# Performance work log

Hardware: AMD Instinct MI355X
Metric: run time of the kernel (lower is better)

Reference implementation:

```python
import jax, jax.numpy as jnp
import numpy as np

B, T, C, H, W = 2, 2048, 2048, 16, 512
D = C // H  # head_dim = 128

def setup_inputs() -> dict:
    key = jax.random.key(0)
    k1, k2, k3 = jax.random.split(key, 3)
    x = jax.random.normal(k1, (B, T, C), dtype=jnp.float32)
    w_attn = jax.random.normal(k2, (C, 3 * C), dtype=jnp.float32) * 0.02
    w_proj = jax.random.normal(k3, (C, C), dtype=jnp.float32) * 0.02
    # standard RoPE tables: [T, D] with halves repeated
    inv_freq = 1.0 / (10000.0 ** (jnp.arange(0, D, 2, dtype=jnp.float32) / D))
    freqs = jnp.outer(jnp.arange(T, dtype=jnp.float32), inv_freq)  # [T, D/2]
    emb = jnp.concatenate([freqs, freqs], axis=-1)  # [T, D]
    return {"x": x, "freqs_cos": jnp.cos(emb), "freqs_sin": jnp.sin(emb),
            "w_attn": w_attn, "w_proj": w_proj}

def _rotate_half(t):
    return jnp.concatenate([-t[..., D // 2:], t[..., :D // 2]], axis=-1)

def reference(x, freqs_cos, freqs_sin, w_attn, w_proj):
    qkv = x @ w_attn  # [B,T,3C]
    q, k, v = jnp.split(qkv, 3, axis=-1)
    # [B,T,C] -> [B,H,T,D]
    q = q.reshape(B, T, H, D).transpose(0, 2, 1, 3)
    k = k.reshape(B, T, H, D).transpose(0, 2, 1, 3)
    v = v.reshape(B, T, H, D).transpose(0, 2, 1, 3)
    cos = freqs_cos[None, None, :, :]  # [1,1,T,D]
    sin = freqs_sin[None, None, :, :]
    q = q * cos + _rotate_half(q) * sin
    k = k * cos + _rotate_half(k) * sin
    scores = jnp.einsum('bhqd,bhkd->bhqk', q, k) / jnp.sqrt(jnp.float32(D))
    i = jnp.arange(T)[:, None]
    j = jnp.arange(T)[None, :]
    band = (j <= i) & (j > i - W)  # causal sliding window of width W
    scores = jnp.where(band[None, None, :, :], scores, -jnp.inf)
    att = jax.nn.softmax(scores, axis=-1)
    y = jnp.einsum('bhqk,bhkd->bhqd', att, v)
    y = y.transpose(0, 2, 1, 3).reshape(B, T, C)
    return y @ w_proj
```

## Files before the change

kernel.cpp:

```cpp
#include <hip/hip_runtime.h>
#include <stdint.h>

#define B_ 2
#define T_ 2048
#define C_ 2048
#define H_ 16
#define D_ 128
#define W_ 512
#define M_ (B_*T_)
#define N1_ (3*C_)

typedef short bf16x8 __attribute__((ext_vector_type(8)));
typedef unsigned short u16x8 __attribute__((ext_vector_type(8)));
typedef float f32x4 __attribute__((ext_vector_type(4)));

#define SB() __builtin_amdgcn_sched_barrier(0)

__device__ __forceinline__ unsigned short f2bf(float f) {
  union { float f; unsigned u; } v; v.f = f;
  unsigned r = v.u + 0x7fffu + ((v.u >> 16) & 1u);
  return (unsigned short)(r >> 16);
}
__device__ __forceinline__ float bf2f(unsigned short b) {
  union { unsigned u; float f; } v; v.u = ((unsigned)b) << 16;
  return v.f;
}

__device__ __forceinline__ void gload_lds16(const void* g, void* l) {
  __builtin_amdgcn_global_load_lds((const __attribute__((address_space(1))) void*)g,
                                   (__attribute__((address_space(3))) void*)l, 16, 0, 0);
}

__global__ void k_cvt(const float* __restrict__ s, unsigned short* __restrict__ d, int n) {
  int i = (blockIdx.x * blockDim.x + threadIdx.x) * 8;
  if (i >= n) return;
  float4 a = *(const float4*)(s + i);
  float4 b = *(const float4*)(s + i + 4);
  u16x8 o;
  o[0]=f2bf(a.x); o[1]=f2bf(a.y); o[2]=f2bf(a.z); o[3]=f2bf(a.w);
  o[4]=f2bf(b.x); o[5]=f2bf(b.y); o[6]=f2bf(b.z); o[7]=f2bf(b.w);
  *(u16x8*)(d + i) = o;
}

__global__ void k_tcvt(const float* __restrict__ s, unsigned short* __restrict__ d, int R, int Cc) {
  __shared__ float tile[32][33];
  int c0 = blockIdx.x * 32, r0 = blockIdx.y * 32;
  int tx = threadIdx.x & 31, ty = threadIdx.x >> 5;
  #pragma unroll
  for (int j = 0; j < 32; j += 8) tile[ty + j][tx] = s[(size_t)(r0 + ty + j) * Cc + c0 + tx];
  __syncthreads();
  #pragma unroll
  for (int j = 0; j < 32; j += 8) d[(size_t)(c0 + ty + j) * R + r0 + tx] = f2bf(tile[tx][ty + j]);
}

template<int ROWS>
__device__ __forceinline__ void stage_half(const unsigned short* __restrict__ gbase,
                                           int row0, int K, int kt, int kh,
                                           unsigned short* region, int tid, int sw) {
  const char* gsrc = (const char*)(gbase + (size_t)row0 * K + kt * 64 + kh * 32);
  {
    int o = tid * 16, s = o ^ sw;
    gload_lds16(gsrc + (size_t)(s >> 6) * (K * 2) + (s & 63), (char*)region + o);
  }
  if (ROWS == 256) {
    int o = (512 + tid) * 16, s = o ^ sw;
    gload_lds16(gsrc + (size_t)(s >> 6) * (K * 2) + (s & 63), (char*)region + o);
  }
}

template<bool F32OUT>
__global__ __launch_bounds__(512, 2) void k_gemm8(const unsigned short* __restrict__ A,
                                                  const unsigned short* __restrict__ Bt,
                                                  void* __restrict__ Cp,
                                                  int Ntot, int K) {
  __shared__ unsigned short As[2][2][256 * 32];
  __shared__ unsigned short Bs[2][2][256 * 32];
  const int tid = threadIdx.x, lane = tid & 63, wv = tid >> 6;
  const int wm = wv >> 2, wn = wv & 3;
  const int lr = lane & 15, lg = lane >> 4;
  const int sw = tid & 32;
  const int fofs = lr * 64 + ((lg * 16) ^ ((lr & 8) << 2));
  const int aoff = wm * 128 * 64 + fofs;
  const int boff = wn * 64 * 64 + fofs;

  const int nwg = gridDim.x;
  const int nbx = Ntot >> 8;
  const int q = nwg >> 3, r = nwg & 7;
  const int xcd = blockIdx.x & 7, off = blockIdx.x >> 3;
  const int bid = (xcd < r ? xcd * (q + 1) : r * (q + 1) + (xcd - r) * q) + off;
  const int bm0 = (bid / nbx) << 8;
  const int bn0 = (bid % nbx) << 8;

  f32x4 acc[8][4];
  #pragma unroll
  for (int i = 0; i < 8; ++i)
    #pragma unroll
    for (int j = 0; j < 4; ++j)
      #pragma unroll
      for (int e = 0; e < 4; ++e) acc[i][j][e] = 0.f;

  const int NT = K >> 6;

  stage_half<256>(A,  bm0, K, 0, 0, As[0][0], tid, sw);
  stage_half<256>(Bt, bn0, K, 0, 0, Bs[0][0], tid, sw);
  stage_half<256>(Bt, bn0, K, 0, 1, Bs[0][1], tid, sw);
  stage_half<256>(A,  bm0, K, 0, 1, As[0][1], tid, sw);
  stage_half<256>(Bt, bn0, K, 1, 0, Bs[1][0], tid, sw);
  stage_half<256>(A,  bm0, K, 1, 0, As[1][0], tid, sw);
  stage_half<256>(Bt, bn0, K, 1, 1, Bs[1][1], tid, sw);
  asm volatile("s_waitcnt vmcnt(4)" ::: "memory");
  __builtin_amdgcn_s_barrier();

  bf16x8 Xa[4], Xb[4], Ya[4];
  #pragma unroll
  for (int j = 0; j < 4; ++j) Xb[j] = *(const bf16x8*)((const char*)Bs[0][0] + boff + j * 1024);
  #pragma unroll
  for (int i = 0; i < 4; ++i) Xa[i] = *(const bf16x8*)((const char*)As[0][0] + aoff + i * 1024);

  #pragma unroll 2
  for (int t = 0; t < NT; ++t) {
    const int p = t & 1;
    asm volatile("s_waitcnt lgkmcnt(0)" ::: "memory");
    __builtin_amdgcn_sched_barrier(0);
    __builtin_amdgcn_s_setprio(1);
    #pragma unroll
    for (int i = 0; i < 4; ++i)
      #pragma unroll
      for (int j = 0; j < 4; ++j)
        acc[i][j] = __builtin_amdgcn_mfma_f32_16x16x32_bf16(Xa[i], Xb[j], acc[i][j], 0, 0, 0);
    __builtin_amdgcn_s_setprio(0);
    #pragma unroll
    for (int i = 0; i < 4; ++i) Ya[i] = *(const bf16x8*)((const char*)As[p][0] + aoff + (i + 4) * 1024);
    if (t + 1 < NT) stage_half<256>(A, bm0, K, t + 1, 1, As[p ^ 1][1], tid, sw);
    __builtin_amdgcn_s_barrier();

    asm volatile("s_waitcnt lgkmcnt(0)" ::: "memory");
    __builtin_amdgcn_sched_barrier(0);
    __builtin_amdgcn_s_setprio(1);
    #pragma unroll
    for (int i = 0; i < 4; ++i)
      #pragma unroll
      for (int j = 0; j < 4; ++j)
        acc[i + 4][j] = __builtin_amdgcn_mfma_f32_16x16x32_bf16(Ya[i], Xb[j], acc[i + 4][j], 0, 0, 0);
    __builtin_amdgcn_s_setprio(0);
    #pragma unroll
    for (int j = 0; j < 4; ++j) Xb[j] = *(const bf16x8*)((const char*)Bs[p][1] + boff + j * 1024);
    #pragma unroll
    for (int i = 0; i < 4; ++i) Xa[i] = *(const bf16x8*)((const char*)As[p][1] + aoff + i * 1024);
    if (t + 2 < NT) stage_half<256>(Bt, bn0, K, t + 2, 0, Bs[p][0], tid, sw);
    __builtin_amdgcn_s_barrier();

    asm volatile("s_waitcnt lgkmcnt(0)" ::: "memory");
    __builtin_amdgcn_sched_barrier(0);
    __builtin_amdgcn_s_setprio(1);
    #pragma unroll
    for (int i = 0; i < 4; ++i)
      #pragma unroll
      for (int j = 0; j < 4; ++j)
        acc[i][j] = __builtin_amdgcn_mfma_f32_16x16x32_bf16(Xa[i], Xb[j], acc[i][j], 0, 0, 0);
    __builtin_amdgcn_s_setprio(0);
    #pragma unroll
    for (int i = 0; i < 4; ++i) Ya[i] = *(const bf16x8*)((const char*)As[p][1] + aoff + (i + 4) * 1024);
    if (t + 2 < NT) stage_half<256>(A, bm0, K, t + 2, 0, As[p][0], tid, sw);
    __builtin_amdgcn_s_barrier();

    asm volatile("s_waitcnt lgkmcnt(0)" ::: "memory");
    __builtin_amdgcn_sched_barrier(0);
    __builtin_amdgcn_s_setprio(1);
    #pragma unroll
    for (int i = 0; i < 4; ++i)
      #pragma unroll
      for (int j = 0; j < 4; ++j)
        acc[i + 4][j] = __builtin_amdgcn_mfma_f32_16x16x32_bf16(Ya[i], Xb[j], acc[i + 4][j], 0, 0, 0);
    __builtin_amdgcn_s_setprio(0);
    if (t < NT - 2) asm volatile("s_waitcnt vmcnt(4)" ::: "memory");
    else            asm volatile("s_waitcnt vmcnt(0)" ::: "memory");
    #pragma unroll
    for (int j = 0; j < 4; ++j) Xb[j] = *(const bf16x8*)((const char*)Bs[p ^ 1][0] + boff + j * 1024);
    #pragma unroll
    for (int i = 0; i < 4; ++i) Xa[i] = *(const bf16x8*)((const char*)As[p ^ 1][0] + aoff + i * 1024);
    if (t + 2 < NT) stage_half<256>(Bt, bn0, K, t + 2, 1, Bs[p][1], tid, sw);
    __builtin_amdgcn_s_barrier();
  }
  asm volatile("s_waitcnt lgkmcnt(0)" ::: "memory");

  #pragma unroll
  for (int i = 0; i < 8; ++i)
    #pragma unroll
    for (int j = 0; j < 4; ++j) {
      int m = bm0 + wm * 128 + i * 16 + lg * 4;
      int n = bn0 + wn * 64 + j * 16 + lr;
      #pragma unroll
      for (int e = 0; e < 4; ++e) {
        if (F32OUT) ((float*)Cp)[(size_t)(m + e) * Ntot + n] = acc[i][j][e];
        else ((unsigned short*)Cp)[(size_t)(m + e) * Ntot + n] = f2bf(acc[i][j][e]);
      }
    }
}

template<bool F32OUT>
__global__ __launch_bounds__(512, 1) void k_gemmT(const unsigned short* __restrict__ A,
                                                  const unsigned short* __restrict__ Bt,
                                                  void* __restrict__ Cp,
                                                  int Ntot, int K) {
  __shared__ unsigned short As[3][2][128 * 32];
  __shared__ unsigned short Bs[3][2][256 * 32];
  const int tid = threadIdx.x, lane = tid & 63, wv = tid >> 6;
  const int wm = wv >> 2, wn = wv & 3;
  const int lr = lane & 15, lg = lane >> 4;
  const int sw = tid & 32;
  const int fofs = lr * 64 + ((lg * 16) ^ ((lr & 8) << 2));
  const int aoff = wm * 64 * 64 + fofs;
  const int boff = wn * 64 * 64 + fofs;

  const int nwg = gridDim.x;
  const int nbx = Ntot >> 8;
  const int q = nwg >> 3, r = nwg & 7;
  const int xcd = blockIdx.x & 7, off = blockIdx.x >> 3;
  const int bid = (xcd < r ? xcd * (q + 1) : r * (q + 1) + (xcd - r) * q) + off;
  const int bm0 = (bid / nbx) * 128;
  const int bn0 = (bid % nbx) << 8;

  f32x4 acc[4][4];
  #pragma unroll
  for (int i = 0; i < 4; ++i)
    #pragma unroll
    for (int j = 0; j < 4; ++j)
      #pragma unroll
      for (int e = 0; e < 4; ++e) acc[i][j][e] = 0.f;

  const int NT = K >> 6;

  auto stage_tile = [&](int kt, int rr) {
    stage_half<128>(A,  bm0, K, kt, 0, As[rr][0], tid, sw);
    stage_half<256>(Bt, bn0, K, kt, 0, Bs[rr][0], tid, sw);
    stage_half<128>(A,  bm0, K, kt, 1, As[rr][1], tid, sw);
    stage_half<256>(Bt, bn0, K, kt, 1, Bs[rr][1], tid, sw);
  };

  stage_tile(0, 0);
  stage_tile(1, 1);
  asm volatile("s_waitcnt vmcnt(6)" ::: "memory");
  __builtin_amdgcn_s_barrier();
  bf16x8 Pf[4], Qf[4], Xf[4], Yf[4];
  #pragma unroll
  for (int i = 0; i < 4; ++i) Pf[i] = *(const bf16x8*)((const char*)As[0][0] + aoff + i * 1024);
  #pragma unroll
  for (int j = 0; j < 4; ++j) Xf[j] = *(const bf16x8*)((const char*)Bs[0][0] + boff + j * 1024);

  int cur = 0;
  for (int t = 0; t < NT; ++t) {
    int rn = cur + 1; if (rn == 3) rn = 0;
    int rs = rn + 1; if (rs == 3) rs = 0;

    asm volatile("s_waitcnt lgkmcnt(0)" ::: "memory");
    SB();
    __builtin_amdgcn_s_setprio(1);
    #pragma unroll
    for (int i = 0; i < 4; ++i)
      #pragma unroll
      for (int j = 0; j < 4; ++j)
        acc[i][j] = __builtin_amdgcn_mfma_f32_16x16x32_bf16(Pf[i], Xf[j], acc[i][j], 0, 0, 0);
    __builtin_amdgcn_s_setprio(0);
    #pragma unroll
    for (int i = 0; i < 4; ++i) Qf[i] = *(const bf16x8*)((const char*)As[cur][1] + aoff + i * 1024);
    #pragma unroll
    for (int j = 0; j < 4; ++j) Yf[j] = *(const bf16x8*)((const char*)Bs[cur][1] + boff + j * 1024);
    if (t + 2 < NT) {
      stage_tile(t + 2, rs);
      asm volatile("s_waitcnt vmcnt(9)" ::: "memory");
    } else if (t + 1 < NT) {
      asm volatile("s_waitcnt vmcnt(3)" ::: "memory");
    } else {
      asm volatile("s_waitcnt vmcnt(0)" ::: "memory");
    }
    __builtin_amdgcn_s_barrier();

    asm volatile("s_waitcnt lgkmcnt(0)" ::: "memory");
    SB();
    __builtin_amdgcn_s_setprio(1);
    #pragma unroll
    for (int i = 0; i < 4; ++i)
      #pragma unroll
      for (int j = 0; j < 4; ++j)
        acc[i][j] = __builtin_amdgcn_mfma_f32_16x16x32_bf16(Qf[i], Yf[j], acc[i][j], 0, 0, 0);
    __builtin_amdgcn_s_setprio(0);
    if (t + 1 < NT) {
      #pragma unroll
      for (int i = 0; i < 4; ++i) Pf[i] = *(const bf16x8*)((const char*)As[rn][0] + aoff + i * 1024);
      #pragma unroll
      for (int j = 0; j < 4; ++j) Xf[j] = *(const bf16x8*)((const char*)Bs[rn][0] + boff + j * 1024);
    }
    if (t + 2 < NT) asm volatile("s_waitcnt vmcnt(6)" ::: "memory");
    else            asm volatile("s_waitcnt vmcnt(0)" ::: "memory");
    __builtin_amdgcn_s_barrier();

    cur = rn;
  }
  asm volatile("s_waitcnt lgkmcnt(0)" ::: "memory");

  #pragma unroll
  for (int i = 0; i < 4; ++i)
    #pragma unroll
    for (int j = 0; j < 4; ++j) {
      int m = bm0 + wm * 64 + i * 16 + lg * 4;
      int n = bn0 + wn * 64 + j * 16 + lr;
      #pragma unroll
      for (int e = 0; e < 4; ++e) {
        if (F32OUT) ((float*)Cp)[(size_t)(m + e) * Ntot + n] = acc[i][j][e];
        else ((unsigned short*)Cp)[(size_t)(m + e) * Ntot + n] = f2bf(acc[i][j][e]);
      }
    }
}

__global__ __launch_bounds__(256) void k_reorg(const unsigned short* __restrict__ qkv,
                        const float* __restrict__ fcos, const float* __restrict__ fsin,
                        unsigned short* __restrict__ q_r, unsigned short* __restrict__ k_r,
                        unsigned short* __restrict__ v_t) {
  const int bh = blockIdx.x, b = bh >> 4, h = bh & 15;
  const int t0 = blockIdx.y * 64;
  const int tid = threadIdx.x;
  __shared__ unsigned short vt[64][136];
  #pragma unroll
  for (int p = 0; p < 4; ++p) {
    int idx = p * 256 + tid;
    int tl = idx >> 4, sg = idx & 15;
    int t = t0 + tl, d0 = sg * 8;
    float sgn = (d0 < 64) ? -1.f : 1.f;
    float4 c0v = *(const float4*)(fcos + t * D_ + d0);
    float4 c1v = *(const float4*)(fcos + t * D_ + d0 + 4);
    float4 s0v = *(const float4*)(fsin + t * D_ + d0);
    float4 s1v = *(const float4*)(fsin + t * D_ + d0 + 4);
    float cs[8] = {c0v.x,c0v.y,c0v.z,c0v.w,c1v.x,c1v.y,c1v.z,c1v.w};
    float sn[8] = {s0v.x,s0v.y,s0v.z,s0v.w,s1v.x,s1v.y,s1v.z,s1v.w};
    #pragma unroll
    for (int w = 0; w < 2; ++w) {
      const unsigned short* src = qkv + (size_t)(b*T_ + t) * N1_ + w*C_ + h*D_;
      u16x8 a  = *(const u16x8*)(src + d0);
      u16x8 pr = *(const u16x8*)(src + (d0 ^ 64));
      u16x8 o;
      #pragma unroll
      for (int e = 0; e < 8; ++e)
        o[e] = f2bf(bf2f(a[e]) * cs[e] + sgn * bf2f(pr[e]) * sn[e]);
      unsigned short* dst = (w ? k_r : q_r) + (size_t)((b*H_ + h)*T_ + t) * D_ + d0;
      *(u16x8*)dst = o;
    }
    const unsigned short* vsrc = qkv + (size_t)(b*T_ + t) * N1_ + 2*C_ + h*D_ + d0;
    *(u16x8*)&vt[tl][d0] = *(const u16x8*)vsrc;
  }
  __syncthreads();
  #pragma unroll
  for (int p = 0; p < 4; ++p) {
    int idx = p * 256 + tid;
    int sg = idx & 7, d = idx >> 3;
    u16x8 o;
    #pragma unroll
    for (int e = 0; e < 8; ++e) o[e] = vt[sg*8 + e][d];
    *(u16x8*)(v_t + (size_t)((b*H_ + h)*D_ + d) * T_ + t0 + sg*8) = o;
  }
}

__global__ __launch_bounds__(512) void k_attn(const unsigned short* __restrict__ q_r,
                       const unsigned short* __restrict__ k_r,
                       const unsigned short* __restrict__ v_t,
                       unsigned short* __restrict__ y) {
  const int bh = blockIdx.x, b = bh >> 4, h = bh & 15;
  const int q0 = blockIdx.y * 128;
  const int tid = threadIdx.x, lane = tid & 63, wv = tid >> 6;
  const int lr = lane & 15, lg = lane >> 4;

  __shared__ unsigned short Ks[2][64 * 128];
  __shared__ unsigned short Vs[2][128 * 64];
  __shared__ unsigned short Ps[8 * 16 * 64];

  const size_t bhT = (size_t)(b*H_ + h) * T_;
  const size_t bhD = (size_t)(b*H_ + h) * D_;
  const unsigned short* qbase = q_r + (bhT + q0 + wv*16 + lr) * D_;
  bf16x8 qf[4];
  #pragma unroll
  for (int kk = 0; kk < 4; ++kk) qf[kk] = *(const bf16x8*)(qbase + kk*32 + lg*8);

  f32x4 o[8];
  #pragma unroll
  for (int i = 0; i < 8; ++i)
    #pragma unroll
    for (int e = 0; e < 4; ++e) o[i][e] = 0.f;
  float m_run[4], l_sum[4];
  #pragma unroll
  for (int e = 0; e < 4; ++e) { m_run[e] = -1e30f; l_sum[e] = 0.f; }

  const int i_min = q0 + wv*16, i_max = i_min + 15;
  int kt_lo = q0 - (W_ - 1); if (kt_lo < 0) kt_lo = 0; kt_lo &= ~63;
  const float scale = 0.08838834764831845f;

  unsigned short* Ps_w = Ps + wv * 1024;

  auto stage_kv = [&](int kt, int buf) {
    #pragma unroll
    for (int c = 0; c < 2; ++c) {
      int ob = (c * 512 + tid) * 16;
      int row = ob >> 8, slot = (ob >> 4) & 15;
      int cb = slot ^ ((row & 7) << 1);
      gload_lds16(k_r + (bhT + kt + row) * D_ + cb * 8, (char*)Ks[buf] + ob);
    }
    #pragma unroll
    for (int c = 0; c < 2; ++c) {
      int ob = (c * 512 + tid) * 16;
      int d = ob >> 7, slot = (ob >> 4) & 7;
      int cb = slot ^ (d & 7);
      gload_lds16(v_t + (bhD + d) * T_ + kt + cb * 8, (char*)Vs[buf] + ob);
    }
  };

  stage_kv(kt_lo, 0);
  int cur = 0;
  for (int kt = kt_lo; kt < q0 + 128; kt += 64) {
    const bool has_next = (kt + 64 < q0 + 128);
    if (has_next) stage_kv(kt + 64, cur ^ 1);
    if (has_next) asm volatile("s_waitcnt vmcnt(4)" ::: "memory");
    else          asm volatile("s_waitcnt vmcnt(0)" ::: "memory");
    __builtin_amdgcn_s_barrier();

    if (kt <= i_max && kt + 63 >= i_min - (W_ - 1)) {
      const unsigned short* Kc = Ks[cur];
      const unsigned short* Vc = Vs[cur];
      f32x4 s[4];
      #pragma unroll
      for (int ct = 0; ct < 4; ++ct)
        #pragma unroll
        for (int e = 0; e < 4; ++e) s[ct][e] = 0.f;
      #pragma unroll
      for (int kk = 0; kk < 4; ++kk) {
        #pragma unroll
        for (int ct = 0; ct < 4; ++ct) {
          bf16x8 kf = *(const bf16x8*)&Kc[(ct*16 + lr)*128 + ((kk*4 + lg) ^ ((lr & 7) << 1))*8];
          s[ct] = __builtin_amdgcn_mfma_f32_16x16x32_bf16(qf[kk], kf, s[ct], 0, 0, 0);
        }
      }
      float sv[4][4], mnew[4];
      int grow = 0;
      #pragma unroll
      for (int e = 0; e < 4; ++e) {
        int i = i_min + lg*4 + e;
        float rm = -1e30f;
        #pragma unroll
        for (int ct = 0; ct < 4; ++ct) {
          int j = kt + ct*16 + lr;
          bool ok = (j <= i) && (j > i - W_);
          sv[e][ct] = ok ? s[ct][e] * scale : -1e30f;
          rm = fmaxf(rm, sv[e][ct]);
        }
        #pragma unroll
        for (int msk = 1; msk < 16; msk <<= 1) rm = fmaxf(rm, __shfl_xor(rm, msk));
        mnew[e] = fmaxf(m_run[e], rm);
        grow |= (mnew[e] > m_run[e]) ? 1 : 0;
      }
      if (__any(grow)) {
        #pragma unroll
        for (int e = 0; e < 4; ++e) {
          float fac = __expf(m_run[e] - mnew[e]);
          l_sum[e] *= fac;
          m_run[e] = mnew[e];
          #pragma unroll
          for (int nt = 0; nt < 8; ++nt) o[nt][e] *= fac;
        }
      }
      #pragma unroll
      for (int e = 0; e < 4; ++e) {
        int prow = lg*4 + e;
        float rs = 0.f;
        #pragma unroll
        for (int ct = 0; ct < 4; ++ct) {
          float pv = (sv[e][ct] > -1e29f) ? __expf(sv[e][ct] - m_run[e]) : 0.f;
          rs += pv;
          Ps_w[prow*64 + ((ct*2 + (lr >> 3)) ^ (prow & 7))*8 + (lr & 7)] = f2bf(pv);
        }
        #pragma unroll
        for (int msk = 1; msk < 16; msk <<= 1) rs += __shfl_xor(rs, msk);
        l_sum[e] += rs;
      }
      asm volatile("s_waitcnt lgkmcnt(0)" ::: "memory"); SB();
      #pragma unroll
      for (int kk = 0; kk < 2; ++kk) {
        bf16x8 pf = *(const bf16x8*)&Ps_w[lr*64 + ((kk*4 + lg) ^ (lr & 7))*8];
        #pragma unroll
        for (int nt = 0; nt < 8; ++nt) {
          bf16x8 vf = *(const bf16x8*)&Vc[(nt*16 + lr)*64 + ((kk*4 + lg) ^ (lr & 7))*8];
          o[nt] = __builtin_amdgcn_mfma_f32_16x16x32_bf16(pf, vf, o[nt], 0, 0, 0);
        }
      }
    }
    asm volatile("s_waitcnt lgkmcnt(0)" ::: "memory");
    __builtin_amdgcn_s_barrier();
    cur ^= 1;
  }

  #pragma unroll
  for (int nt = 0; nt < 8; ++nt) {
    #pragma unroll
    for (int e = 0; e < 4; ++e) {
      int t = q0 + wv*16 + lg*4 + e;
      int d = nt*16 + lr;
      y[(size_t)(b*T_ + t) * C_ + h*D_ + d] = f2bf(o[nt][e] / l_sum[e]);
    }
  }
}

extern "C" void kernel_launch(void* const* d_in, const int* in_sizes, int n_in,
                              void* d_out, int out_size, void* d_ws, size_t ws_size,
                              hipStream_t stream) {
  const float* x      = (const float*)d_in[0];
  const float* fcos   = (const float*)d_in[1];
  const float* fsin   = (const float*)d_in[2];
  const float* w_attn = (const float*)d_in[3];
  const float* w_proj = (const float*)d_in[4];
  float* out = (float*)d_out;

  char* ws = (char*)d_ws;
  unsigned short* x_bf = (unsigned short*)(ws);
  unsigned short* wa_t = (unsigned short*)(ws + 16777216ull);
  unsigned short* wp_t = (unsigned short*)(ws + 41943040ull);
  unsigned short* qkv  = (unsigned short*)(ws + 50331648ull);
  unsigned short* q_r  = (unsigned short*)(ws + 100663296ull);
  unsigned short* k_r  = (unsigned short*)(ws + 117440512ull);
  unsigned short* v_t  = (unsigned short*)(ws + 134217728ull);
  unsigned short* y_bf = x_bf;

  k_cvt<<<dim3(4096), dim3(256), 0, stream>>>(x, x_bf, M_*C_);
  k_tcvt<<<dim3(192, 64), dim3(256), 0, stream>>>(w_attn, wa_t, C_, N1_);
  k_tcvt<<<dim3(64, 64), dim3(256), 0, stream>>>(w_proj, wp_t, C_, C_);
  k_gemm8<false><<<dim3(384), dim3(512), 0, stream>>>(x_bf, wa_t, qkv, N1_, C_);
  k_reorg<<<dim3(32, 32), dim3(256), 0, stream>>>(qkv, fcos, fsin, q_r, k_r, v_t);
  k_attn<<<dim3(32, 16), dim3(512), 0, stream>>>(q_r, k_r, v_t, y_bf);
  k_gemmT<true><<<dim3(256), dim3(512), 0, stream>>>(y_bf, wp_t, out, C_, C_);
}
```

Before: 290.3 us.

## Retile QKV GEMM to 256x192 tiles and single-buffer V in attention

The QKV projection GEMM now uses 256x192 output tiles, giving 512 workgroups instead of 384, so the 256 CUs divide the work evenly without a partial second wave. B-tile staging uses 4-byte global-to-LDS loads with adjusted vmcnt waits. The attention kernel single-buffers V and stages it just before use, with an extra barrier between the QK/softmax and PV phases, to reduce LDS footprint. Trade-offs are smaller, less efficient 4-byte loads and an extra synchronization per KV tile in attention.

```diff
diff --git a/kernel.cpp b/kernel.cpp
--- a/kernel.cpp
+++ b/kernel.cpp
@@ -29,6 +29,10 @@
 __device__ __forceinline__ void gload_lds16(const void* g, void* l) {
   __builtin_amdgcn_global_load_lds((const __attribute__((address_space(1))) void*)g,
                                    (__attribute__((address_space(3))) void*)l, 16, 0, 0);
+}
+__device__ __forceinline__ void gload_lds4(const void* g, void* l) {
+  __builtin_amdgcn_global_load_lds((const __attribute__((address_space(1))) void*)g,
+                                   (__attribute__((address_space(3))) void*)l, 4, 0, 0);
 }
 
 __global__ void k_cvt(const float* __restrict__ s, unsigned short* __restrict__ d, int n) {
@@ -67,53 +71,63 @@
     gload_lds16(gsrc + (size_t)(s >> 6) * (K * 2) + (s & 63), (char*)region + o);
   }
 }
-
-template<bool F32OUT>
-__global__ __launch_bounds__(512, 2) void k_gemm8(const unsigned short* __restrict__ A,
-                                                  const unsigned short* __restrict__ Bt,
-                                                  void* __restrict__ Cp,
-                                                  int Ntot, int K) {
+__device__ __forceinline__ void stage_b192(const unsigned short* __restrict__ gbase,
+                                           int row0, int K, int kt, int kh,
+                                           unsigned short* region, int tid) {
+  const char* gsrc = (const char*)(gbase + (size_t)row0 * K + kt * 64 + kh * 32);
+  #pragma unroll
+  for (int tk = 0; tk < 6; ++tk) {
+    int o = tk * 2048 + tid * 4;
+    int s = o ^ (((o >> 9) & 1) << 5);
+    gload_lds4(gsrc + (size_t)(s >> 6) * (K * 2) + (s & 63), (char*)region + o);
+  }
+}
+
+__global__ __launch_bounds__(512, 2) void k_gemm192(const unsigned short* __restrict__ A,
+                                                    const unsigned short* __restrict__ Bt,
+                                                    unsigned short* __restrict__ Cp,
+                                                    int Ntot, int K) {
   __shared__ unsigned short As[2][2][256 * 32];
-  __shared__ unsigned short Bs[2][2][256 * 32];
+  __shared__ unsigned short Bs[2][2][192 * 32];
   const int tid = threadIdx.x, lane = tid & 63, wv = tid >> 6;
   const int wm = wv >> 2, wn = wv & 3;
   const int lr = lane & 15, lg = lane >> 4;
   const int sw = tid & 32;
   const int fofs = lr * 64 + ((lg * 16) ^ ((lr & 8) << 2));
   const int aoff = wm * 128 * 64 + fofs;
-  const int boff = wn * 64 * 64 + fofs;
+  const int boff = wn * 48 * 64 + fofs;
 
   const int nwg = gridDim.x;
-  const int nbx = Ntot >> 8;
+  const int nbx = Ntot / 192;
   const int q = nwg >> 3, r = nwg & 7;
   const int xcd = blockIdx.x & 7, off = blockIdx.x >> 3;
   const int bid = (xcd < r ? xcd * (q + 1) : r * (q + 1) + (xcd - r) * q) + off;
   const int bm0 = (bid / nbx) << 8;
-  const int bn0 = (bid % nbx) << 8;
-
-  f32x4 acc[8][4];
+  const int bn0 = (bid % nbx) * 192;
+
+  f32x4 acc[8][3];
   #pragma unroll
   for (int i = 0; i < 8; ++i)
     #pragma unroll
-    for (int j = 0; j < 4; ++j)
+    for (int j = 0; j < 3; ++j)
       #pragma unroll
       for (int e = 0; e < 4; ++e) acc[i][j][e] = 0.f;
 
   const int NT = K >> 6;
 
   stage_half<256>(A,  bm0, K, 0, 0, As[0][0], tid, sw);
-  stage_half<256>(Bt, bn0, K, 0, 0, Bs[0][0], tid, sw);
-  stage_half<256>(Bt, bn0, K, 0, 1, Bs[0][1], tid, sw);
+  stage_b192(Bt, bn0, K, 0, 0, Bs[0][0], tid);
+  stage_b192(Bt, bn0, K, 0, 1, Bs[0][1], tid);
   stage_half<256>(A,  bm0, K, 0, 1, As[0][1], tid, sw);
-  stage_half<256>(Bt, bn0, K, 1, 0, Bs[1][0], tid, sw);
+  stage_b192(Bt, bn0, K, 1, 0, Bs[1][0], tid);
   stage_half<256>(A,  bm0, K, 1, 0, As[1][0], tid, sw);
-  stage_half<256>(Bt, bn0, K, 1, 1, Bs[1][1], tid, sw);
-  asm volatile("s_waitcnt vmcnt(4)" ::: "memory");
+  stage_b192(Bt, bn0, K, 1, 1, Bs[1][1], tid);
+  asm volatile("s_waitcnt vmcnt(8)" ::: "memory");
   __builtin_amdgcn_s_barrier();
 
-  bf16x8 Xa[4], Xb[4], Ya[4];
-  #pragma unroll
-  for (int j = 0; j < 4; ++j) Xb[j] = *(const bf16x8*)((const char*)Bs[0][0] + boff + j * 1024);
+  bf16x8 Xa[4], Xb[3], Ya[4];
+  #pragma unroll
+  for (int j = 0; j < 3; ++j) Xb[j] = *(const bf16x8*)((const char*)Bs[0][0] + boff + j * 1024);
   #pragma unroll
   for (int i = 0; i < 4; ++i) Xa[i] = *(const bf16x8*)((const char*)As[0][0] + aoff + i * 1024);
 
@@ -121,12 +135,12 @@
   for (int t = 0; t < NT; ++t) {
     const int p = t & 1;
     asm volatile("s_waitcnt lgkmcnt(0)" ::: "memory");
-    __builtin_amdgcn_sched_barrier(0);
+    SB();
     __builtin_amdgcn_s_setprio(1);
     #pragma unroll
     for (int i = 0; i < 4; ++i)
       #pragma unroll
-      for (int j = 0; j < 4; ++j)
+      for (int j = 0; j < 3; ++j)
         acc[i][j] = __builtin_amdgcn_mfma_f32_16x16x32_bf16(Xa[i], Xb[j], acc[i][j], 0, 0, 0);
     __builtin_amdgcn_s_setprio(0);
     #pragma unroll
@@ -135,28 +149,28 @@
     __builtin_amdgcn_s_barrier();
 
     asm volatile("s_waitcnt lgkmcnt(0)" ::: "memory");
-    __builtin_amdgcn_sched_barrier(0);
+    SB();
     __builtin_amdgcn_s_setprio(1);
     #pragma unroll
     for (int i = 0; i < 4; ++i)
       #pragma unroll
-      for (int j = 0; j < 4; ++j)
+      for (int j = 0; j < 3; ++j)
         acc[i + 4][j] = __builtin_amdgcn_mfma_f32_16x16x32_bf16(Ya[i], Xb[j], acc[i + 4][j], 0, 0, 0);
     __builtin_amdgcn_s_setprio(0);
     #pragma unroll
-    for (int j = 0; j < 4; ++j) Xb[j] = *(const bf16x8*)((const char*)Bs[p][1] + boff + j * 1024);
+    for (int j = 0; j < 3; ++j) Xb[j] = *(const bf16x8*)((const char*)Bs[p][1] + boff + j * 1024);
     #pragma unroll
     for (int i = 0; i < 4; ++i) Xa[i] = *(const bf16x8*)((const char*)As[p][1] + aoff + i * 1024);
-    if (t + 2 < NT) stage_half<256>(Bt, bn0, K, t + 2, 0, Bs[p][0], tid, sw);
-    __builtin_amdgcn_s_barrier();
-
-    asm volatile("s_waitcnt lgkmcnt(0)" ::: "memory");
-    __builtin_amdgcn_sched_barrier(0);
+    if (t + 2 < NT) stage_b192(Bt, bn0, K, t + 2, 0, Bs[p][0], tid);
+    __builtin_amdgcn_s_barrier();
+
+    asm volatile("s_waitcnt lgkmcnt(0)" ::: "memory");
+    SB();
     __builtin_amdgcn_s_setprio(1);
     #pragma unroll
     for (int i = 0; i < 4; ++i)
       #pragma unroll
-      for (int j = 0; j < 4; ++j)
+      for (int j = 0; j < 3; ++j)
         acc[i][j] = __builtin_amdgcn_mfma_f32_16x16x32_bf16(Xa[i], Xb[j], acc[i][j], 0, 0, 0);
     __builtin_amdgcn_s_setprio(0);
     #pragma unroll
@@ -165,21 +179,21 @@
     __builtin_amdgcn_s_barrier();
 
     asm volatile("s_waitcnt lgkmcnt(0)" ::: "memory");
-    __builtin_amdgcn_sched_barrier(0);
+    SB();
     __builtin_amdgcn_s_setprio(1);
     #pragma unroll
     for (int i = 0; i < 4; ++i)
       #pragma unroll
-      for (int j = 0; j < 4; ++j)
+      for (int j = 0; j < 3; ++j)
         acc[i + 4][j] = __builtin_amdgcn_mfma_f32_16x16x32_bf16(Ya[i], Xb[j], acc[i + 4][j], 0, 0, 0);
     __builtin_amdgcn_s_setprio(0);
-    if (t < NT - 2) asm volatile("s_waitcnt vmcnt(4)" ::: "memory");
+    if (t < NT - 2) asm volatile("s_waitcnt vmcnt(8)" ::: "memory");
     else            asm volatile("s_waitcnt vmcnt(0)" ::: "memory");
     #pragma unroll
-    for (int j = 0; j < 4; ++j) Xb[j] = *(const bf16x8*)((const char*)Bs[p ^ 1][0] + boff + j * 1024);
+    for (int j = 0; j < 3; ++j) Xb[j] = *(const bf16x8*)((const char*)Bs[p ^ 1][0] + boff + j * 1024);
     #pragma unroll
     for (int i = 0; i < 4; ++i) Xa[i] = *(const bf16x8*)((const char*)As[p ^ 1][0] + aoff + i * 1024);
-    if (t + 2 < NT) stage_half<256>(Bt, bn0, K, t + 2, 1, Bs[p][1], tid, sw);
+    if (t + 2 < NT) stage_b192(Bt, bn0, K, t + 2, 1, Bs[p][1], tid);
     __builtin_amdgcn_s_barrier();
   }
   asm volatile("s_waitcnt lgkmcnt(0)" ::: "memory");
@@ -187,14 +201,12 @@
   #pragma unroll
   for (int i = 0; i < 8; ++i)
     #pragma unroll
-    for (int j = 0; j < 4; ++j) {
+    for (int j = 0; j < 3; ++j) {
       int m = bm0 + wm * 128 + i * 16 + lg * 4;
-      int n = bn0 + wn * 64 + j * 16 + lr;
-      #pragma unroll
-      for (int e = 0; e < 4; ++e) {
-        if (F32OUT) ((float*)Cp)[(size_t)(m + e) * Ntot + n] = acc[i][j][e];
-        else ((unsigned short*)Cp)[(size_t)(m + e) * Ntot + n] = f2bf(acc[i][j][e]);
-      }
+      int n = bn0 + wn * 48 + j * 16 + lr;
+      #pragma unroll
+      for (int e = 0; e < 4; ++e)
+        Cp[(size_t)(m + e) * Ntot + n] = f2bf(acc[i][j][e]);
     }
 }
 
@@ -370,7 +382,7 @@
   const int lr = lane & 15, lg = lane >> 4;
 
   __shared__ unsigned short Ks[2][64 * 128];
-  __shared__ unsigned short Vs[2][128 * 64];
+  __shared__ unsigned short Vs[128 * 64];
   __shared__ unsigned short Ps[8 * 16 * 64];
 
   const size_t bhT = (size_t)(b*H_ + h) * T_;
@@ -395,7 +407,7 @@
 
   unsigned short* Ps_w = Ps + wv * 1024;
 
-  auto stage_kv = [&](int kt, int buf) {
+  auto stage_k = [&](int kt, int buf) {
     #pragma unroll
     for (int c = 0; c < 2; ++c) {
       int ob = (c * 512 + tid) * 16;
@@ -403,27 +415,31 @@
       int cb = slot ^ ((row & 7) << 1);
       gload_lds16(k_r + (bhT + kt + row) * D_ + cb * 8, (char*)Ks[buf] + ob);
     }
+  };
+  auto stage_v = [&](int kt) {
     #pragma unroll
     for (int c = 0; c < 2; ++c) {
       int ob = (c * 512 + tid) * 16;
       int d = ob >> 7, slot = (ob >> 4) & 7;
       int cb = slot ^ (d & 7);
-      gload_lds16(v_t + (bhD + d) * T_ + kt + cb * 8, (char*)Vs[buf] + ob);
+      gload_lds16(v_t + (bhD + d) * T_ + kt + cb * 8, (char*)Vs + ob);
     }
   };
 
-  stage_kv(kt_lo, 0);
+  stage_k(kt_lo, 0);
   int cur = 0;
   for (int kt = kt_lo; kt < q0 + 128; kt += 64) {
     const bool has_next = (kt + 64 < q0 + 128);
-    if (has_next) stage_kv(kt + 64, cur ^ 1);
+    stage_v(kt);
+    if (has_next) stage_k(kt + 64, cur ^ 1);
     if (has_next) asm volatile("s_waitcnt vmcnt(4)" ::: "memory");
-    else          asm volatile("s_waitcnt vmcnt(0)" ::: "memory");
-    __builtin_amdgcn_s_barrier();
-
-    if (kt <= i_max && kt + 63 >= i_min - (W_ - 1)) {
+    else          asm volatile("s_waitcnt vmcnt(2)" ::: "memory");
+    __builtin_amdgcn_s_barrier();
+
+    const bool live = (kt <= i_max) && (kt + 63 >= i_min - (W_ - 1));
+    float sv[4][4];
+    if (live) {
       const unsigned short* Kc = Ks[cur];
-      const unsigned short* Vc = Vs[cur];
       f32x4 s[4];
       #pragma unroll
       for (int ct = 0; ct < 4; ++ct)
@@ -437,7 +453,7 @@
           s[ct] = __builtin_amdgcn_mfma_f32_16x16x32_bf16(qf[kk], kf, s[ct], 0, 0, 0);
         }
       }
-      float sv[4][4], mnew[4];
+      float mnew[4];
       int grow = 0;
       #pragma unroll
       for (int e = 0; e < 4; ++e) {
@@ -479,13 +495,19 @@
         for (int msk = 1; msk < 16; msk <<= 1) rs += __shfl_xor(rs, msk);
         l_sum[e] += rs;
       }
+    }
+    if (has_next) asm volatile("s_waitcnt vmcnt(2)" ::: "memory");
+    else          asm volatile("s_waitcnt vmcnt(0)" ::: "memory");
+    __builtin_amdgcn_s_barrier();
+
+    if (live) {
       asm volatile("s_waitcnt lgkmcnt(0)" ::: "memory"); SB();
       #pragma unroll
       for (int kk = 0; kk < 2; ++kk) {
         bf16x8 pf = *(const bf16x8*)&Ps_w[lr*64 + ((kk*4 + lg) ^ (lr & 7))*8];
         #pragma unroll
         for (int nt = 0; nt < 8; ++nt) {
-          bf16x8 vf = *(const bf16x8*)&Vc[(nt*16 + lr)*64 + ((kk*4 + lg) ^ (lr & 7))*8];
+          bf16x8 vf = *(const bf16x8*)&Vs[(nt*16 + lr)*64 + ((kk*4 + lg) ^ (lr & 7))*8];
           o[nt] = __builtin_amdgcn_mfma_f32_16x16x32_bf16(pf, vf, o[nt], 0, 0, 0);
         }
       }
@@ -529,7 +551,7 @@
   k_cvt<<<dim3(4096), dim3(256), 0, stream>>>(x, x_bf, M_*C_);
   k_tcvt<<<dim3(192, 64), dim3(256), 0, stream>>>(w_attn, wa_t, C_, N1_);
   k_tcvt<<<dim3(64, 64), dim3(256), 0, stream>>>(w_proj, wp_t, C_, C_);
-  k_gemm8<false><<<dim3(384), dim3(512), 0, stream>>>(x_bf, wa_t, qkv, N1_, C_);
+  k_gemm192<<<dim3(512), dim3(512), 0, stream>>>(x_bf, wa_t, qkv, N1_, C_);
   k_reorg<<<dim3(32, 32), dim3(256), 0, stream>>>(qkv, fcos, fsin, q_r, k_r, v_t);
   k_attn<<<dim3(32, 16), dim3(512), 0, stream>>>(q_r, k_r, v_t, y_bf);
   k_gemmT<true><<<dim3(256), dim3(512), 0, stream>>>(y_bf, wp_t, out, C_, C_);
```

New measurement: 288.2 us. About the same (-0.7%).

## Template GEMM sizes and split K/V staging in attention to single-buffer V

Applied to the files above, without the earlier changes.

The GEMM kernels now take K and Ntot as template parameters, so address arithmetic and loop trip counts are known at compile time. In the attention kernel, V moves from a double buffer to a single buffer that is staged each iteration, and the loop gains a second wait-and-barrier between QK/softmax and PV. This cuts LDS use, which may raise occupancy, and lets the V load overlap the score computation. The cost is an extra barrier per tile and less prefetch lead for V.

```diff
diff --git a/kernel.cpp b/kernel.cpp
--- a/kernel.cpp
+++ b/kernel.cpp
@@ -53,9 +53,9 @@
   for (int j = 0; j < 32; j += 8) d[(size_t)(c0 + ty + j) * R + r0 + tx] = f2bf(tile[tx][ty + j]);
 }
 
-template<int ROWS>
+template<int ROWS, int K>
 __device__ __forceinline__ void stage_half(const unsigned short* __restrict__ gbase,
-                                           int row0, int K, int kt, int kh,
+                                           int row0, int kt, int kh,
                                            unsigned short* region, int tid, int sw) {
   const char* gsrc = (const char*)(gbase + (size_t)row0 * K + kt * 64 + kh * 32);
   {
@@ -68,11 +68,10 @@
   }
 }
 
-template<bool F32OUT>
+template<bool F32OUT, int K, int Ntot>
 __global__ __launch_bounds__(512, 2) void k_gemm8(const unsigned short* __restrict__ A,
                                                   const unsigned short* __restrict__ Bt,
-                                                  void* __restrict__ Cp,
-                                                  int Ntot, int K) {
+                                                  void* __restrict__ Cp) {
   __shared__ unsigned short As[2][2][256 * 32];
   __shared__ unsigned short Bs[2][2][256 * 32];
   const int tid = threadIdx.x, lane = tid & 63, wv = tid >> 6;
@@ -99,15 +98,15 @@
       #pragma unroll
       for (int e = 0; e < 4; ++e) acc[i][j][e] = 0.f;
 
-  const int NT = K >> 6;
-
-  stage_half<256>(A,  bm0, K, 0, 0, As[0][0], tid, sw);
-  stage_half<256>(Bt, bn0, K, 0, 0, Bs[0][0], tid, sw);
-  stage_half<256>(Bt, bn0, K, 0, 1, Bs[0][1], tid, sw);
-  stage_half<256>(A,  bm0, K, 0, 1, As[0][1], tid, sw);
-  stage_half<256>(Bt, bn0, K, 1, 0, Bs[1][0], tid, sw);
-  stage_half<256>(A,  bm0, K, 1, 0, As[1][0], tid, sw);
-  stage_half<256>(Bt, bn0, K, 1, 1, Bs[1][1], tid, sw);
+  constexpr int NT = K >> 6;
+
+  stage_half<256, K>(A,  bm0, 0, 0, As[0][0], tid, sw);
+  stage_half<256, K>(Bt, bn0, 0, 0, Bs[0][0], tid, sw);
+  stage_half<256, K>(Bt, bn0, 0, 1, Bs[0][1], tid, sw);
+  stage_half<256, K>(A,  bm0, 0, 1, As[0][1], tid, sw);
+  stage_half<256, K>(Bt, bn0, 1, 0, Bs[1][0], tid, sw);
+  stage_half<256, K>(A,  bm0, 1, 0, As[1][0], tid, sw);
+  stage_half<256, K>(Bt, bn0, 1, 1, Bs[1][1], tid, sw);
   asm volatile("s_waitcnt vmcnt(4)" ::: "memory");
   __builtin_amdgcn_s_barrier();
 
@@ -121,7 +120,7 @@
   for (int t = 0; t < NT; ++t) {
     const int p = t & 1;
     asm volatile("s_waitcnt lgkmcnt(0)" ::: "memory");
-    __builtin_amdgcn_sched_barrier(0);
+    SB();
     __builtin_amdgcn_s_setprio(1);
     #pragma unroll
     for (int i = 0; i < 4; ++i)
@@ -131,11 +130,11 @@
     __builtin_amdgcn_s_setprio(0);
     #pragma unroll
     for (int i = 0; i < 4; ++i) Ya[i] = *(const bf16x8*)((const char*)As[p][0] + aoff + (i + 4) * 1024);
-    if (t + 1 < NT) stage_half<256>(A, bm0, K, t + 1, 1, As[p ^ 1][1], tid, sw);
-    __builtin_amdgcn_s_barrier();
-
-    asm volatile("s_waitcnt lgkmcnt(0)" ::: "memory");
-    __builtin_amdgcn_sched_barrier(0);
+    if (t + 1 < NT) stage_half<256, K>(A, bm0, t + 1, 1, As[p ^ 1][1], tid, sw);
+    __builtin_amdgcn_s_barrier();
+
+    asm volatile("s_waitcnt lgkmcnt(0)" ::: "memory");
+    SB();
     __builtin_amdgcn_s_setprio(1);
     #pragma unroll
     for (int i = 0; i < 4; ++i)
@@ -147,11 +146,11 @@
     for (int j = 0; j < 4; ++j) Xb[j] = *(const bf16x8*)((const char*)Bs[p][1] + boff + j * 1024);
     #pragma unroll
     for (int i = 0; i < 4; ++i) Xa[i] = *(const bf16x8*)((const char*)As[p][1] + aoff + i * 1024);
-    if (t + 2 < NT) stage_half<256>(Bt, bn0, K, t + 2, 0, Bs[p][0], tid, sw);
-    __builtin_amdgcn_s_barrier();
-
-    asm volatile("s_waitcnt lgkmcnt(0)" ::: "memory");
-    __builtin_amdgcn_sched_barrier(0);
+    if (t + 2 < NT) stage_half<256, K>(Bt, bn0, t + 2, 0, Bs[p][0], tid, sw);
+    __builtin_amdgcn_s_barrier();
+
+    asm volatile("s_waitcnt lgkmcnt(0)" ::: "memory");
+    SB();
     __builtin_amdgcn_s_setprio(1);
     #pragma unroll
     for (int i = 0; i < 4; ++i)
@@ -161,11 +160,11 @@
     __builtin_amdgcn_s_setprio(0);
     #pragma unroll
     for (int i = 0; i < 4; ++i) Ya[i] = *(const bf16x8*)((const char*)As[p][1] + aoff + (i + 4) * 1024);
-    if (t + 2 < NT) stage_half<256>(A, bm0, K, t + 2, 0, As[p][0], tid, sw);
-    __builtin_amdgcn_s_barrier();
-
-    asm volatile("s_waitcnt lgkmcnt(0)" ::: "memory");
-    __builtin_amdgcn_sched_barrier(0);
+    if (t + 2 < NT) stage_half<256, K>(A, bm0, t + 2, 0, As[p][0], tid, sw);
+    __builtin_amdgcn_s_barrier();
+
+    asm volatile("s_waitcnt lgkmcnt(0)" ::: "memory");
+    SB();
     __builtin_amdgcn_s_setprio(1);
     #pragma unroll
     for (int i = 0; i < 4; ++i)
@@ -179,7 +178,7 @@
     for (int j = 0; j < 4; ++j) Xb[j] = *(const bf16x8*)((const char*)Bs[p ^ 1][0] + boff + j * 1024);
     #pragma unroll
     for (int i = 0; i < 4; ++i) Xa[i] = *(const bf16x8*)((const char*)As[p ^ 1][0] + aoff + i * 1024);
-    if (t + 2 < NT) stage_half<256>(Bt, bn0, K, t + 2, 1, Bs[p][1], tid, sw);
+    if (t + 2 < NT) stage_half<256, K>(Bt, bn0, t + 2, 1, Bs[p][1], tid, sw);
     __builtin_amdgcn_s_barrier();
   }
   asm volatile("s_waitcnt lgkmcnt(0)" ::: "memory");
@@ -198,11 +197,10 @@
     }
 }
 
-template<bool F32OUT>
+template<bool F32OUT, int K, int Ntot>
 __global__ __launch_bounds__(512, 1) void k_gemmT(const unsigned short* __restrict__ A,
                                                   const unsigned short* __restrict__ Bt,
-                                                  void* __restrict__ Cp,
-                                                  int Ntot, int K) {
+                                                  void* __restrict__ Cp) {
   __shared__ unsigned short As[3][2][128 * 32];
   __shared__ unsigned short Bs[3][2][256 * 32];
   const int tid = threadIdx.x, lane = tid & 63, wv = tid >> 6;
@@ -229,13 +227,13 @@
       #pragma unroll
       for (int e = 0; e < 4; ++e) acc[i][j][e] = 0.f;
 
-  const int NT = K >> 6;
+  constexpr int NT = K >> 6;
 
   auto stage_tile = [&](int kt, int rr) {
-    stage_half<128>(A,  bm0, K, kt, 0, As[rr][0], tid, sw);
-    stage_half<256>(Bt, bn0, K, kt, 0, Bs[rr][0], tid, sw);
-    stage_half<128>(A,  bm0, K, kt, 1, As[rr][1], tid, sw);
-    stage_half<256>(Bt, bn0, K, kt, 1, Bs[rr][1], tid, sw);
+    stage_half<128, K>(A,  bm0, kt, 0, As[rr][0], tid, sw);
+    stage_half<256, K>(Bt, bn0, kt, 0, Bs[rr][0], tid, sw);
+    stage_half<128, K>(A,  bm0, kt, 1, As[rr][1], tid, sw);
+    stage_half<256, K>(Bt, bn0, kt, 1, Bs[rr][1], tid, sw);
   };
 
   stage_tile(0, 0);
@@ -370,7 +368,7 @@
   const int lr = lane & 15, lg = lane >> 4;
 
   __shared__ unsigned short Ks[2][64 * 128];
-  __shared__ unsigned short Vs[2][128 * 64];
+  __shared__ unsigned short Vs[128 * 64];
   __shared__ unsigned short Ps[8 * 16 * 64];
 
   const size_t bhT = (size_t)(b*H_ + h) * T_;
@@ -395,7 +393,7 @@
 
   unsigned short* Ps_w = Ps + wv * 1024;
 
-  auto stage_kv = [&](int kt, int buf) {
+  auto stage_k = [&](int kt, int buf) {
     #pragma unroll
     for (int c = 0; c < 2; ++c) {
       int ob = (c * 512 + tid) * 16;
@@ -403,27 +401,31 @@
       int cb = slot ^ ((row & 7) << 1);
       gload_lds16(k_r + (bhT + kt + row) * D_ + cb * 8, (char*)Ks[buf] + ob);
     }
+  };
+  auto stage_v = [&](int kt) {
     #pragma unroll
     for (int c = 0; c < 2; ++c) {
       int ob = (c * 512 + tid) * 16;
       int d = ob >> 7, slot = (ob >> 4) & 7;
       int cb = slot ^ (d & 7);
-      gload_lds16(v_t + (bhD + d) * T_ + kt + cb * 8, (char*)Vs[buf] + ob);
+      gload_lds16(v_t + (bhD + d) * T_ + kt + cb * 8, (char*)Vs + ob);
     }
   };
 
-  stage_kv(kt_lo, 0);
+  stage_k(kt_lo, 0);
   int cur = 0;
   for (int kt = kt_lo; kt < q0 + 128; kt += 64) {
     const bool has_next = (kt + 64 < q0 + 128);
-    if (has_next) stage_kv(kt + 64, cur ^ 1);
+    stage_v(kt);
+    if (has_next) stage_k(kt + 64, cur ^ 1);
     if (has_next) asm volatile("s_waitcnt vmcnt(4)" ::: "memory");
-    else          asm volatile("s_waitcnt vmcnt(0)" ::: "memory");
-    __builtin_amdgcn_s_barrier();
-
-    if (kt <= i_max && kt + 63 >= i_min - (W_ - 1)) {
+    else          asm volatile("s_waitcnt vmcnt(2)" ::: "memory");
+    __builtin_amdgcn_s_barrier();
+
+    const bool live = (kt <= i_max) && (kt + 63 >= i_min - (W_ - 1));
+    float sv[4][4];
+    if (live) {
       const unsigned short* Kc = Ks[cur];
-      const unsigned short* Vc = Vs[cur];
       f32x4 s[4];
       #pragma unroll
       for (int ct = 0; ct < 4; ++ct)
@@ -437,7 +439,7 @@
           s[ct] = __builtin_amdgcn_mfma_f32_16x16x32_bf16(qf[kk], kf, s[ct], 0, 0, 0);
         }
       }
-      float sv[4][4], mnew[4];
+      float mnew[4];
       int grow = 0;
       #pragma unroll
       for (int e = 0; e < 4; ++e) {
@@ -479,13 +481,19 @@
         for (int msk = 1; msk < 16; msk <<= 1) rs += __shfl_xor(rs, msk);
         l_sum[e] += rs;
       }
+    }
+    if (has_next) asm volatile("s_waitcnt vmcnt(2)" ::: "memory");
+    else          asm volatile("s_waitcnt vmcnt(0)" ::: "memory");
+    __builtin_amdgcn_s_barrier();
+
+    if (live) {
       asm volatile("s_waitcnt lgkmcnt(0)" ::: "memory"); SB();
       #pragma unroll
       for (int kk = 0; kk < 2; ++kk) {
         bf16x8 pf = *(const bf16x8*)&Ps_w[lr*64 + ((kk*4 + lg) ^ (lr & 7))*8];
         #pragma unroll
         for (int nt = 0; nt < 8; ++nt) {
-          bf16x8 vf = *(const bf16x8*)&Vc[(nt*16 + lr)*64 + ((kk*4 + lg) ^ (lr & 7))*8];
+          bf16x8 vf = *(const bf16x8*)&Vs[(nt*16 + lr)*64 + ((kk*4 + lg) ^ (lr & 7))*8];
           o[nt] = __builtin_amdgcn_mfma_f32_16x16x32_bf16(pf, vf, o[nt], 0, 0, 0);
         }
       }
@@ -529,8 +537,8 @@
   k_cvt<<<dim3(4096), dim3(256), 0, stream>>>(x, x_bf, M_*C_);
   k_tcvt<<<dim3(192, 64), dim3(256), 0, stream>>>(w_attn, wa_t, C_, N1_);
   k_tcvt<<<dim3(64, 64), dim3(256), 0, stream>>>(w_proj, wp_t, C_, C_);
-  k_gemm8<false><<<dim3(384), dim3(512), 0, stream>>>(x_bf, wa_t, qkv, N1_, C_);
+  k_gemm8<false, C_, N1_><<<dim3(384), dim3(512), 0, stream>>>(x_bf, wa_t, qkv);
   k_reorg<<<dim3(32, 32), dim3(256), 0, stream>>>(qkv, fcos, fsin, q_r, k_r, v_t);
   k_attn<<<dim3(32, 16), dim3(512), 0, stream>>>(q_r, k_r, v_t, y_bf);
-  k_gemmT<true><<<dim3(256), dim3(512), 0, stream>>>(y_bf, wp_t, out, C_, C_);
-}
+  k_gemmT<true, C_, C_><<<dim3(256), dim3(512), 0, stream>>>(y_bf, wp_t, out);
+}
```

Measured after the change: 283.3 us. 1.02x faster.
